# Kernel tuning notes

Measured on AMD Instinct MI355X. Metric: run time of the kernel, lower is better.

The kernel has to match this reference:

```python
import jax, jax.numpy as jnp
import numpy as np

D_MODEL = 512
KEY_DIM = 512
VALUE_DIM = 512
N_HEADS = 8


def setup_inputs() -> dict:
    key = jax.random.key(0)
    ks = jax.random.split(key, 12)
    B, S = 8, 1024
    s = 0.02
    return {
        "input1": jax.random.normal(ks[0], (B, S, D_MODEL), jnp.float32),
        "input2": jax.random.normal(ks[1], (B, S, D_MODEL), jnp.float32),
        "input3": jax.random.normal(ks[2], (B, S, D_MODEL), jnp.float32),
        # per-head projection weights stacked over heads: [H, D, d]
        "Wq": jax.random.normal(ks[3], (N_HEADS, D_MODEL, KEY_DIM), jnp.float32) * s,
        "bq": jnp.zeros((N_HEADS, KEY_DIM), jnp.float32),
        "Wk": jax.random.normal(ks[4], (N_HEADS, D_MODEL, KEY_DIM), jnp.float32) * s,
        "bk": jnp.zeros((N_HEADS, KEY_DIM), jnp.float32),
        "Wv": jax.random.normal(ks[5], (N_HEADS, D_MODEL, VALUE_DIM), jnp.float32) * s,
        "bv": jnp.zeros((N_HEADS, VALUE_DIM), jnp.float32),
        # output projection: concat of heads (H*VALUE_DIM) -> KEY_DIM
        "Wo": jax.random.normal(ks[6], (N_HEADS * VALUE_DIM, KEY_DIM), jnp.float32) * s,
        "bo": jnp.zeros((KEY_DIM,), jnp.float32),
    }


def reference(input1, input2, input3, Wq, bq, Wk, bk, Wv, bv, Wo, bo):
    # Batched equivalent of the per-head Python loop:
    # each head: q=Dense_q(input1), k=Dense_k(input2), v=Dense_v(input3);
    # softmax(q k^T / sqrt(key_dim)) v; concat over heads; Dense w_o.
    q = jnp.einsum("bsd,hde->bhse", input1, Wq) + bq[None, :, None, :]
    k = jnp.einsum("bsd,hde->bhse", input2, Wk) + bk[None, :, None, :]
    v = jnp.einsum("bsd,hde->bhse", input3, Wv) + bv[None, :, None, :]
    scale = 1.0 / jnp.sqrt(jnp.asarray(KEY_DIM, q.dtype))
    scores = jnp.einsum("bhqe,bhke->bhqk", q, k) * scale  # [B,H,S,S]
    attn = jax.nn.softmax(scores, axis=-1)
    heads = jnp.einsum("bhqk,bhke->bhqe", attn, v)  # [B,H,S,VALUE_DIM]
    B, H, S, E = heads.shape
    concat = jnp.transpose(heads, (0, 2, 1, 3)).reshape(B, S, H * E)
    return concat @ Wo + bo
```

## Files before the change

kernel.cpp:

```cpp
#include <hip/hip_runtime.h>
#include <hip/hip_bf16.h>

#define DEV static __device__ __forceinline__

typedef float f32x4 __attribute__((ext_vector_type(4)));
typedef __bf16 b16x8 __attribute__((ext_vector_type(8)));

DEV unsigned short f2bf(float f) {
  union { __hip_bfloat16 h; unsigned short u; } cv;
  cv.h = __float2bfloat16(f);
  return cv.u;
}

DEV void gload_lds16(const unsigned short* g, unsigned short* l) {
  __builtin_amdgcn_global_load_lds(
      (__attribute__((address_space(1))) void*)g,
      (__attribute__((address_space(3))) void*)l, 16, 0, 0);
}

__global__ __launch_bounds__(256) void k_conv_bf16(const float* __restrict__ src,
                                                   unsigned short* __restrict__ dst,
                                                   long long n4) {
  long long i = (long long)blockIdx.x * 256 + threadIdx.x;
  if (i >= n4) return;
  const float4 v = ((const float4*)src)[i];
  ushort4 o;
  o.x = f2bf(v.x); o.y = f2bf(v.y); o.z = f2bf(v.z); o.w = f2bf(v.w);
  ((ushort4*)dst)[i] = o;
}

__global__ __launch_bounds__(256) void k_transpose_bf16(const float* __restrict__ src,
                                                        unsigned short* __restrict__ dst,
                                                        int R, int C) {
  __shared__ float t[32][33];
  const long long zo = (long long)blockIdx.z * R * C;
  const int c0 = blockIdx.x * 32, r0 = blockIdx.y * 32;
  const int tx = threadIdx.x, ty = threadIdx.y;
#pragma unroll
  for (int i = 0; i < 4; ++i)
    t[ty + i * 8][tx] = src[zo + (long long)(r0 + ty + i * 8) * C + c0 + tx];
  __syncthreads();
#pragma unroll
  for (int i = 0; i < 4; ++i)
    dst[zo + (long long)(c0 + ty + i * 8) * R + r0 + tx] = f2bf(t[tx][ty + i * 8]);
}

__global__ __launch_bounds__(256) void k_uv(const float* __restrict__ Wq, const float* __restrict__ bk,
                                            const float* __restrict__ Wk, const float* __restrict__ bq,
                                            float* __restrict__ u, float* __restrict__ v) {
  const int sel = blockIdx.y;
  const float* W = sel ? Wk : Wq;
  const float* bb = sel ? bq : bk;
  float* dst = sel ? v : u;
  const int wave = threadIdx.x >> 6, lane = threadIdx.x & 63;
  const int idx = blockIdx.x * 4 + wave;
  const int h = idx >> 9, d = idx & 511;
  const float* wr = W + ((long long)h * 512 + d) * 512 + lane * 8;
  const float* br = bb + h * 512 + lane * 8;
  float s = 0.f;
#pragma unroll
  for (int k = 0; k < 8; ++k) s += wr[k] * br[k];
#pragma unroll
  for (int off = 32; off; off >>= 1) s += __shfl_xor(s, off);
  if (lane == 0) dst[h * 512 + d] = s;
}

__global__ __launch_bounds__(512) void k_bdot(const float* __restrict__ bq,
                                              const float* __restrict__ bk,
                                              float* __restrict__ c) {
  const int wave = threadIdx.x >> 6, lane = threadIdx.x & 63;
  const float* a = bq + wave * 512 + lane * 8;
  const float* b = bk + wave * 512 + lane * 8;
  float s = 0.f;
#pragma unroll
  for (int k = 0; k < 8; ++k) s += a[k] * b[k];
#pragma unroll
  for (int off = 32; off; off >>= 1) s += __shfl_xor(s, off);
  if (lane == 0) c[wave] = s;
}

__global__ __launch_bounds__(256) void k_rtct(const float* __restrict__ in1, const float* __restrict__ in2,
                                              const float* __restrict__ u, const float* __restrict__ v,
                                              const float* __restrict__ cbuf,
                                              float* __restrict__ rt, float* __restrict__ ct) {
  const int sel = blockIdx.y;
  const float* src = sel ? in2 : in1;
  const float* vec = sel ? v : u;
  float* dst = sel ? ct : rt;
  const int row = blockIdx.x;
  __shared__ float x[512];
  const float* p = src + (long long)row * 512;
  x[threadIdx.x] = p[threadIdx.x];
  x[threadIdx.x + 256] = p[threadIdx.x + 256];
  __syncthreads();
  const int wave = threadIdx.x >> 6, lane = threadIdx.x & 63;
  const int b = row >> 10, i = row & 1023;
#pragma unroll
  for (int t = 0; t < 2; ++t) {
    const int h = wave * 2 + t;
    const float* wv = vec + h * 512;
    float s = 0.f;
#pragma unroll
    for (int k = 0; k < 8; ++k) s += x[lane + k * 64] * wv[lane + k * 64];
#pragma unroll
    for (int off = 32; off; off >>= 1) s += __shfl_xor(s, off);
    if (lane == 0)
      dst[((long long)(b * 8 + h)) * 1024 + i] = s + (sel ? 0.f : cbuf[h]);
  }
}

__global__ __launch_bounds__(256) void k_softmax_bf16(unsigned short* __restrict__ P) {
  const int wave = threadIdx.x >> 6, lane = threadIdx.x & 63;
  unsigned short* p = P + ((long long)blockIdx.x * 4 + wave) * 1024 + lane * 16;
  const b16x8 v0 = *(const b16x8*)p;
  const b16x8 v1 = *(const b16x8*)(p + 8);
  float f[16];
#pragma unroll
  for (int j = 0; j < 8; ++j) { f[j] = (float)v0[j]; f[8 + j] = (float)v1[j]; }
  float mx = f[0];
#pragma unroll
  for (int j = 1; j < 16; ++j) mx = fmaxf(mx, f[j]);
#pragma unroll
  for (int off = 32; off; off >>= 1) mx = fmaxf(mx, __shfl_xor(mx, off));
  float sum = 0.f;
#pragma unroll
  for (int j = 0; j < 16; ++j) { f[j] = __expf(f[j] - mx); sum += f[j]; }
#pragma unroll
  for (int off = 32; off; off >>= 1) sum += __shfl_xor(sum, off);
  const float inv = 1.f / sum;
  b16x8 o0, o1;
#pragma unroll
  for (int j = 0; j < 8; ++j) { o0[j] = (__bf16)(f[j] * inv); o1[j] = (__bf16)(f[8 + j] * inv); }
  *(b16x8*)p = o0;
  *(b16x8*)(p + 8) = o1;
}

template <int OM>
__global__ __launch_bounds__(256) void k_gemm_bt(
    const unsigned short* __restrict__ A, const unsigned short* __restrict__ Bt,
    void* __restrict__ Cv, const float* __restrict__ bias,
    const float* __restrict__ rAdd, const float* __restrict__ cAdd,
    int K, int lda, int ldb, int ldc,
    int azs, int azm, long long azr,
    int bzs, int bzm, long long bzr,
    int czs, long long czr, int czm, int czc,
    int biasm, int bstr, int rstr, float scale) {
  __shared__ unsigned short lA[128 * 64];
  __shared__ unsigned short lB[128 * 64];
  const int tid = threadIdx.x, wave = tid >> 6, lane = tid & 63;
  const int z = blockIdx.z;
  const int m0 = blockIdx.y * 128, n0 = blockIdx.x * 128;
  const unsigned short* Az = A + (long long)((z >> azs) & azm) * azr + (long long)m0 * lda;
  const unsigned short* Bz = Bt + (long long)((z >> bzs) & bzm) * bzr + (long long)n0 * ldb;

  const int srow = wave * 32 + (lane >> 3);
  const int scol = (lane & 7) * 8;
  const unsigned short* ga = Az + (long long)srow * lda + scol;
  const unsigned short* gb = Bz + (long long)srow * ldb + scol;
  unsigned short* laBase = &lA[(wave * 32) * 64];
  unsigned short* lbBase = &lB[(wave * 32) * 64];

  f32x4 acc[4][4] = {};
  const int wr = (wave >> 1) * 64, wc = (wave & 1) * 64;
  const int fr = lane & 15, kq = (lane >> 4) * 8;

  for (int k0 = 0; k0 < K; k0 += 64) {
#pragma unroll
    for (int i = 0; i < 4; ++i) {
      gload_lds16(ga + (long long)(i * 8) * lda + k0, laBase + (i * 8) * 64);
      gload_lds16(gb + (long long)(i * 8) * ldb + k0, lbBase + (i * 8) * 64);
    }
    __syncthreads();
#pragma unroll
    for (int kk = 0; kk < 64; kk += 32) {
      b16x8 af[4], bf[4];
#pragma unroll
      for (int i = 0; i < 4; ++i)
        af[i] = *(const b16x8*)&lA[(wr + i * 16 + fr) * 64 + kk + kq];
#pragma unroll
      for (int j = 0; j < 4; ++j)
        bf[j] = *(const b16x8*)&lB[(wc + j * 16 + fr) * 64 + kk + kq];
#pragma unroll
      for (int i = 0; i < 4; ++i)
#pragma unroll
        for (int j = 0; j < 4; ++j)
          acc[i][j] = __builtin_amdgcn_mfma_f32_16x16x32_bf16(af[i], bf[j], acc[i][j], 0, 0, 0);
    }
    __syncthreads();
  }

  const long long coff = (long long)(z >> czs) * czr + (long long)(z & czm) * czc;
  const long long zr = (long long)z * rstr;
  const int rr = (lane >> 4) * 4;
#pragma unroll
  for (int j = 0; j < 4; ++j) {
    const int col = n0 + wc + j * 16 + fr;
    const float bval = bias ? bias[(long long)(z & biasm) * bstr + col] : 0.f;
    const float ca = cAdd ? cAdd[zr + col] : 0.f;
#pragma unroll
    for (int i = 0; i < 4; ++i) {
#pragma unroll
      for (int r = 0; r < 4; ++r) {
        const int row = m0 + wr + i * 16 + rr + r;
        const float ra = rAdd ? rAdd[zr + row] : 0.f;
        const float val = (acc[i][j][r] + ra + ca) * scale + bval;
        if constexpr (OM == 1) {
          ((unsigned short*)Cv)[coff + (long long)row * ldc + col] = f2bf(val);
        } else if constexpr (OM == 2) {
          ((unsigned short*)Cv)[coff + (long long)col * ldc + row] = f2bf(val);
        } else {
          ((float*)Cv)[coff + (long long)row * ldc + col] = val;
        }
      }
    }
  }
}

#define STAGE_A8(nb, koff, i)                                  \
  gload_lds16(gaL + (long long)((i) * 8) * lda + (koff) + scol, \
              &sh[nb][(wid * 32 + (i) * 8) * 64])
#define STAGE_B8(nb, koff, i)                                  \
  gload_lds16(gbL + (long long)((i) * 8) * ldb + (koff) + scol, \
              &sh[2 + (nb)][(wid * 32 + (i) * 8) * 64])

template <int OM>
__global__ __launch_bounds__(512, 2) void k_gemm8p(
    const unsigned short* __restrict__ A, const unsigned short* __restrict__ Bt,
    void* __restrict__ Cv, const float* __restrict__ bias,
    const float* __restrict__ rAdd, const float* __restrict__ cAdd,
    int K, int lda, int ldb, int ldc,
    int azs, int azm, long long azr,
    int bzs, int bzm, long long bzr,
    int czs, long long czr, int czm, int czc,
    int biasm, int bstr, int rstr, float scale, int kzm, int kzr) {
  __shared__ unsigned short sh[4][256 * 64];
  const int tid = threadIdx.x, wid = tid >> 6, lane = tid & 63;
  const int wm = wid >> 2, wn = wid & 3;

  const int gx = gridDim.x, gy = gridDim.y;
  const int nwg = gx * gy * gridDim.z;
  const int bidL = blockIdx.x + gx * (blockIdx.y + gy * blockIdx.z);
  const int q8 = nwg >> 3;
  const int idx = (bidL & 7) * q8 + (bidL >> 3);
  const int bx = idx % gx;
  const int rem = idx / gx;
  const int by = rem % gy;
  const int z = rem / gy;

  const int m0 = by * 256, n0 = bx * 256;
  const int kstart = (z & kzm) * kzr;
  const unsigned short* Az = A + (long long)((z >> azs) & azm) * azr + (long long)m0 * lda + kstart;
  const unsigned short* Bz = Bt + (long long)((z >> bzs) & bzm) * bzr + (long long)n0 * ldb + kstart;

  const int scol = (((lane & 7) ^ ((lane >> 3) & 7)) << 3);
  const unsigned short* gaL = Az + (long long)(wid * 32 + (lane >> 3)) * lda;
  const unsigned short* gbL = Bz + (long long)(wid * 32 + (lane >> 3)) * ldb;

  const int fr = lane & 15, kq = (lane >> 4) * 8;
  const int fsw = (fr & 7) << 3;
  const int rc0 = kq ^ fsw;
  const int rc1 = (32 + kq) ^ fsw;
  const int aBase = (wm * 128 + fr) * 64;
  const int bBase = (wn * 64 + fr) * 64;

  f32x4 acc[8][4] = {};
  b16x8 afr[4][2], bfr[4][2];
  const int NT = K >> 6;

#pragma unroll
  for (int i = 0; i < 4; ++i) { STAGE_A8(0, 0, i); STAGE_B8(0, 0, i); }

  for (int kt = 0; kt < NT; ++kt) {
    const int cur = kt & 1, nb = cur ^ 1;
    if (kt + 1 < NT) {
      const int ko = (kt + 1) << 6;
#pragma unroll
      for (int i = 0; i < 4; ++i) { STAGE_A8(nb, ko, i); STAGE_B8(nb, ko, i); }
      asm volatile("s_waitcnt vmcnt(8)" ::: "memory");
    } else {
      asm volatile("s_waitcnt vmcnt(0)" ::: "memory");
    }
    __builtin_amdgcn_s_barrier();
    __builtin_amdgcn_sched_barrier(0);

#pragma unroll
    for (int i = 0; i < 4; ++i) {
      afr[i][0] = *(const b16x8*)&sh[cur][aBase + i * 1024 + rc0];
      afr[i][1] = *(const b16x8*)&sh[cur][aBase + i * 1024 + rc1];
    }
#pragma unroll
    for (int j = 0; j < 2; ++j) {
      bfr[j][0] = *(const b16x8*)&sh[2 + cur][bBase + j * 1024 + rc0];
      bfr[j][1] = *(const b16x8*)&sh[2 + cur][bBase + j * 1024 + rc1];
    }
    __builtin_amdgcn_s_setprio(1);
#pragma unroll
    for (int t = 0; t < 2; ++t)
#pragma unroll
      for (int i = 0; i < 4; ++i)
#pragma unroll
        for (int j = 0; j < 2; ++j)
          acc[i][j] = __builtin_amdgcn_mfma_f32_16x16x32_bf16(afr[i][t], bfr[j][t], acc[i][j], 0, 0, 0);
    __builtin_amdgcn_s_setprio(0);
#pragma unroll
    for (int j = 2; j < 4; ++j) {
      bfr[j][0] = *(const b16x8*)&sh[2 + cur][bBase + j * 1024 + rc0];
      bfr[j][1] = *(const b16x8*)&sh[2 + cur][bBase + j * 1024 + rc1];
    }
    __builtin_amdgcn_s_setprio(1);
#pragma unroll
    for (int t = 0; t < 2; ++t)
#pragma unroll
      for (int i = 0; i < 4; ++i)
#pragma unroll
        for (int j = 2; j < 4; ++j)
          acc[i][j] = __builtin_amdgcn_mfma_f32_16x16x32_bf16(afr[i][t], bfr[j][t], acc[i][j], 0, 0, 0);
    __builtin_amdgcn_s_setprio(0);
#pragma unroll
    for (int i = 0; i < 4; ++i) {
      afr[i][0] = *(const b16x8*)&sh[cur][aBase + (i + 4) * 1024 + rc0];
      afr[i][1] = *(const b16x8*)&sh[cur][aBase + (i + 4) * 1024 + rc1];
    }
    __builtin_amdgcn_s_setprio(1);
#pragma unroll
    for (int t = 0; t < 2; ++t)
#pragma unroll
      for (int i = 0; i < 4; ++i)
#pragma unroll
        for (int j = 0; j < 2; ++j)
          acc[i + 4][j] = __builtin_amdgcn_mfma_f32_16x16x32_bf16(afr[i][t], bfr[j][t], acc[i + 4][j], 0, 0, 0);
    __builtin_amdgcn_s_setprio(0);
    __builtin_amdgcn_s_setprio(1);
#pragma unroll
    for (int t = 0; t < 2; ++t)
#pragma unroll
      for (int i = 0; i < 4; ++i)
#pragma unroll
        for (int j = 2; j < 4; ++j)
          acc[i + 4][j] = __builtin_amdgcn_mfma_f32_16x16x32_bf16(afr[i][t], bfr[j][t], acc[i + 4][j], 0, 0, 0);
    __builtin_amdgcn_s_setprio(0);

    __builtin_amdgcn_s_barrier();
  }

  const long long coff = (long long)(z >> czs) * czr + (long long)(z & czm) * czc;
  const long long zr = (long long)z * rstr;
  const int rr = (lane >> 4) * 4;
  unsigned short* flat = &sh[0][0];

  if constexpr (OM == 1 || OM == 2) {
#pragma unroll
    for (int j = 0; j < 4; ++j) {
      const int col = n0 + wn * 64 + j * 16 + fr;
      const float bval = bias ? bias[(long long)(z & biasm) * bstr + col] : 0.f;
      const float ca = cAdd ? cAdd[zr + col] : 0.f;
#pragma unroll
      for (int i = 0; i < 8; ++i) {
#pragma unroll
        for (int r = 0; r < 4; ++r) {
          const int row = m0 + wm * 128 + i * 16 + rr + r;
          const float ra = rAdd ? rAdd[zr + row] : 0.f;
          const float val = (acc[i][j][r] + ra + ca) * scale + bval;
          const int rowL = wm * 128 + i * 16 + rr + r;
          const int colL = wn * 64 + j * 16 + fr;
          const int sR = (OM == 2) ? colL : rowL;
          const int sC = (OM == 2) ? rowL : colL;
          flat[sR * 256 + (sC ^ ((sR & 7) << 3))] = f2bf(val);
        }
      }
    }
    __builtin_amdgcn_s_barrier();
    const long long rbase = (OM == 2) ? (long long)n0 : (long long)m0;
    const long long cbase = (OM == 2) ? (long long)m0 : (long long)n0;
    unsigned short* Cb = (unsigned short*)Cv;
#pragma unroll
    for (int it = 0; it < 16; ++it) {
      const int t = it * 512 + tid;
      const int R = t >> 5;
      const int Cq = t & 31;
      const int q = Cq ^ (R & 7);
      const b16x8 v = *(const b16x8*)&flat[R * 256 + q * 8];
      *(b16x8*)(Cb + coff + (rbase + R) * ldc + cbase + Cq * 8) = v;
    }
  } else {
    float* fflat = (float*)flat;
    float* Cf = (float*)Cv;
#pragma unroll
    for (int half = 0; half < 2; ++half) {
      if (wm == half) {
#pragma unroll
        for (int j = 0; j < 4; ++j) {
          const int col = n0 + wn * 64 + j * 16 + fr;
          const float bval = bias ? bias[(long long)(z & biasm) * bstr + col] : 0.f;
          const float ca = cAdd ? cAdd[zr + col] : 0.f;
#pragma unroll
          for (int i = 0; i < 8; ++i) {
#pragma unroll
            for (int r = 0; r < 4; ++r) {
              const int row = m0 + wm * 128 + i * 16 + rr + r;
              const float ra = rAdd ? rAdd[zr + row] : 0.f;
              const float val = (acc[i][j][r] + ra + ca) * scale + bval;
              const int Rl = i * 16 + rr + r;
              const int Cl = wn * 64 + j * 16 + fr;
              fflat[Rl * 256 + (Cl ^ ((Rl & 7) << 2))] = val;
            }
          }
        }
      }
      __builtin_amdgcn_s_barrier();
#pragma unroll
      for (int it = 0; it < 16; ++it) {
        const int t = it * 512 + tid;
        const int R = t >> 6;
        const int Cq = t & 63;
        const int q = Cq ^ (R & 7);
        const float4 v = *(const float4*)&fflat[R * 256 + q * 4];
        *(float4*)(Cf + coff + (long long)(m0 + half * 128 + R) * ldc + n0 + Cq * 4) = v;
      }
      __builtin_amdgcn_s_barrier();
    }
  }
}

__global__ __launch_bounds__(256) void k_reduce4(const float* __restrict__ p,
                                                 const float* __restrict__ bo,
                                                 float* __restrict__ out) {
  const long long i = (long long)blockIdx.x * 256 + threadIdx.x;
  const float4* p4 = (const float4*)p;
  float4 a = p4[i], b = p4[i + 1048576], c = p4[i + 2097152], d = p4[i + 3145728];
  const float4 bb = ((const float4*)bo)[i & 127];
  float4 o;
  o.x = a.x + b.x + c.x + d.x + bb.x;
  o.y = a.y + b.y + c.y + d.y + bb.y;
  o.z = a.z + b.z + c.z + d.z + bb.z;
  o.w = a.w + b.w + c.w + d.w + bb.w;
  ((float4*)out)[i] = o;
}

extern "C" void kernel_launch(void* const* d_in, const int* in_sizes, int n_in,
                              void* d_out, int out_size, void* d_ws, size_t ws_size,
                              hipStream_t stream) {
  const float* in1 = (const float*)d_in[0];
  const float* in2 = (const float*)d_in[1];
  const float* in3 = (const float*)d_in[2];
  const float* Wq = (const float*)d_in[3];
  const float* bq = (const float*)d_in[4];
  const float* Wk = (const float*)d_in[5];
  const float* bk = (const float*)d_in[6];
  const float* Wv = (const float*)d_in[7];
  const float* bv = (const float*)d_in[8];
  const float* Wo = (const float*)d_in[9];
  const float* bo = (const float*)d_in[10];

  const long long MB = 1024 * 1024;
  typedef unsigned short us;
  unsigned char* w = (unsigned char*)d_ws;
  us* in2b = (us*)(w);
  us* Tbuf = (us*)(w + 8 * MB);
  us* Vt = (us*)(w + 72 * MB);
  us* wvt = (us*)(w + 136 * MB);
  us* wot = (us*)(w + 140 * MB);
  us* scb = (us*)(w + 144 * MB);
  us* in1b = (us*)(w + 208 * MB);
  us* in3b = (us*)(w + 216 * MB);
  us* wqb = (us*)(w + 224 * MB);
  us* wkb = (us*)(w + 228 * MB);
  us* Gt = (us*)(w + 232 * MB);
  float* rt = (float*)(w + 236 * MB);
  float* ct = (float*)(w + 236 * MB + (256 << 10));
  float* ubuf = (float*)(w + 237 * MB);
  float* vbuf = (float*)(w + 237 * MB + (16 << 10));
  float* cbuf = (float*)(w + 237 * MB + (32 << 10));
  float* partials = (float*)(w + 72 * MB);
  if ((long long)ws_size < 238 * MB) return;

  const float iscale = 0.04419417382415922f;
  const long long SD = 1024 * 512;

  k_conv_bf16<<<4096, 256, 0, stream>>>(in1, in1b, 1048576);
  k_conv_bf16<<<4096, 256, 0, stream>>>(in2, in2b, 1048576);
  k_conv_bf16<<<4096, 256, 0, stream>>>(in3, in3b, 1048576);
  k_conv_bf16<<<2048, 256, 0, stream>>>(Wq, wqb, 524288);
  k_conv_bf16<<<2048, 256, 0, stream>>>(Wk, wkb, 524288);
  k_transpose_bf16<<<dim3(16, 16, 8), dim3(32, 8), 0, stream>>>(Wv, wvt, 512, 512);
  k_transpose_bf16<<<dim3(16, 128, 1), dim3(32, 8), 0, stream>>>(Wo, wot, 4096, 512);

  k_uv<<<dim3(1024, 2), 256, 0, stream>>>(Wq, bk, Wk, bq, ubuf, vbuf);
  k_bdot<<<1, 512, 0, stream>>>(bq, bk, cbuf);
  k_rtct<<<dim3(8192, 2), 256, 0, stream>>>(in1, in2, ubuf, vbuf, cbuf, rt, ct);

  k_gemm_bt<1><<<dim3(4, 4, 8), 256, 0, stream>>>(
      wkb, wqb, Gt, nullptr, nullptr, nullptr, 512, 512, 512, 512,
      0, 7, 262144LL, 0, 7, 262144LL, 0, 262144LL, 0, 0, 0, 0, 0, 1.f);

  k_gemm8p<1><<<dim3(2, 4, 64), 512, 0, stream>>>(
      in1b, Gt, Tbuf, nullptr, nullptr, nullptr, 512, 512, 512, 512,
      3, 7, SD, 0, 7, 262144LL, 0, SD, 0, 0, 0, 0, 0, 1.f, 0, 0);

  k_gemm8p<2><<<dim3(2, 4, 64), 512, 0, stream>>>(
      in3b, wvt, Vt, bv, nullptr, nullptr, 512, 512, 512, 1024,
      3, 7, SD, 0, 7, 262144LL, 0, SD, 0, 0, 7, 512, 0, 1.f, 0, 0);

  for (int c = 0; c < 2; ++c) {
    k_gemm8p<1><<<dim3(4, 4, 32), 512, 0, stream>>>(
        Tbuf + (long long)c * 32 * SD, in2b + (long long)c * 4 * SD, scb, nullptr,
        rt + c * 32768, ct + c * 32768, 512, 512, 512, 1024,
        0, 31, SD, 3, 3, SD, 0, 1048576LL, 0, 0, 0, 0, 1024, iscale, 0, 0);
    k_softmax_bf16<<<8192, 256, 0, stream>>>(scb);
    k_gemm8p<1><<<dim3(2, 4, 32), 512, 0, stream>>>(
        scb, Vt + (long long)c * 32 * SD, Tbuf + (long long)c * 16777216LL, nullptr,
        nullptr, nullptr, 1024, 1024, 1024, 4096,
        0, 31, 1048576LL, 0, 31, SD, 3, 4194304LL, 7, 512, 0, 0, 0, 1.f, 0, 0);
  }

  k_gemm8p<0><<<dim3(2, 32, 4), 512, 0, stream>>>(
      Tbuf, wot, partials, nullptr, nullptr, nullptr, 1024, 4096, 4096, 512,
      0, 0, 0, 0, 0, 0, 0, 4194304LL, 0, 0, 0, 0, 0, 1.f, 3, 1024);
  k_reduce4<<<4096, 256, 0, stream>>>(partials, bo, (float*)d_out);
}
```

Measured before the change: 481.5 us.

## Fold Wo into per-head value projection and fuse PV with output projection

```diff
diff --git a/kernel.cpp b/kernel.cpp
--- a/kernel.cpp
+++ b/kernel.cpp
@@ -107,6 +107,24 @@
     if (lane == 0)
       dst[((long long)(b * 8 + h)) * 1024 + i] = s + (sel ? 0.f : cbuf[h]);
   }
+}
+
+__global__ __launch_bounds__(256) void k_bvo(const float* __restrict__ Wo,
+                                             const float* __restrict__ bv,
+                                             float* __restrict__ bvo) {
+  const int h = blockIdx.x;
+  __shared__ float bs[512];
+  bs[threadIdx.x] = bv[h * 512 + threadIdx.x];
+  bs[threadIdx.x + 256] = bv[h * 512 + threadIdx.x + 256];
+  __syncthreads();
+  float a0 = 0.f, a1 = 0.f;
+  for (int e = 0; e < 512; ++e) {
+    const float* row = Wo + ((long long)(h * 512 + e)) * 512;
+    a0 += bs[e] * row[threadIdx.x];
+    a1 += bs[e] * row[threadIdx.x + 256];
+  }
+  bvo[h * 512 + threadIdx.x] = a0;
+  bvo[h * 512 + threadIdx.x + 256] = a1;
 }
 
 __global__ __launch_bounds__(256) void k_softmax_bf16(unsigned short* __restrict__ P) {
@@ -422,18 +440,18 @@
   }
 }
 
-__global__ __launch_bounds__(256) void k_reduce4(const float* __restrict__ p,
+__global__ __launch_bounds__(256) void k_reduce8(const float* __restrict__ p,
                                                  const float* __restrict__ bo,
                                                  float* __restrict__ out) {
   const long long i = (long long)blockIdx.x * 256 + threadIdx.x;
   const float4* p4 = (const float4*)p;
-  float4 a = p4[i], b = p4[i + 1048576], c = p4[i + 2097152], d = p4[i + 3145728];
   const float4 bb = ((const float4*)bo)[i & 127];
-  float4 o;
-  o.x = a.x + b.x + c.x + d.x + bb.x;
-  o.y = a.y + b.y + c.y + d.y + bb.y;
-  o.z = a.z + b.z + c.z + d.z + bb.z;
-  o.w = a.w + b.w + c.w + d.w + bb.w;
+  float4 o = bb;
+#pragma unroll
+  for (int ks = 0; ks < 8; ++ks) {
+    const float4 v = p4[i + (long long)ks * 524288];
+    o.x += v.x; o.y += v.y; o.z += v.z; o.w += v.w;
+  }
   ((float4*)out)[i] = o;
 }
 
@@ -455,23 +473,25 @@
   const long long MB = 1024 * 1024;
   typedef unsigned short us;
   unsigned char* w = (unsigned char*)d_ws;
-  us* in2b = (us*)(w);
-  us* Tbuf = (us*)(w + 8 * MB);
-  us* Vt = (us*)(w + 72 * MB);
-  us* wvt = (us*)(w + 136 * MB);
-  us* wot = (us*)(w + 140 * MB);
-  us* scb = (us*)(w + 144 * MB);
-  us* in1b = (us*)(w + 208 * MB);
-  us* in3b = (us*)(w + 216 * MB);
-  us* wqb = (us*)(w + 224 * MB);
-  us* wkb = (us*)(w + 228 * MB);
+  us* scb = (us*)(w);
+  float* partials = (float*)(w + 64 * MB);
+  us* Ubuf = (us*)(w + 128 * MB);
+  us* Tc = (us*)(w + 160 * MB);
+  us* in1b = (us*)(w + 192 * MB);
+  us* in2b = (us*)(w + 200 * MB);
+  us* in3b = (us*)(w + 208 * MB);
+  us* wqb = (us*)(w + 216 * MB);
+  us* wkb = (us*)(w + 220 * MB);
+  us* wvb = (us*)(w + 224 * MB);
+  us* wotb = (us*)(w + 228 * MB);
   us* Gt = (us*)(w + 232 * MB);
+  us* Wvot = (us*)(w + 216 * MB);
   float* rt = (float*)(w + 236 * MB);
   float* ct = (float*)(w + 236 * MB + (256 << 10));
-  float* ubuf = (float*)(w + 237 * MB);
-  float* vbuf = (float*)(w + 237 * MB + (16 << 10));
-  float* cbuf = (float*)(w + 237 * MB + (32 << 10));
-  float* partials = (float*)(w + 72 * MB);
+  float* ubuf = (float*)(w + 236 * MB + (512 << 10));
+  float* vbuf = (float*)(w + 236 * MB + (528 << 10));
+  float* cbuf = (float*)(w + 236 * MB + (544 << 10));
+  float* bvo = (float*)(w + 236 * MB + (560 << 10));
   if ((long long)ws_size < 238 * MB) return;
 
   const float iscale = 0.04419417382415922f;
@@ -482,8 +502,8 @@
   k_conv_bf16<<<4096, 256, 0, stream>>>(in3, in3b, 1048576);
   k_conv_bf16<<<2048, 256, 0, stream>>>(Wq, wqb, 524288);
   k_conv_bf16<<<2048, 256, 0, stream>>>(Wk, wkb, 524288);
-  k_transpose_bf16<<<dim3(16, 16, 8), dim3(32, 8), 0, stream>>>(Wv, wvt, 512, 512);
-  k_transpose_bf16<<<dim3(16, 128, 1), dim3(32, 8), 0, stream>>>(Wo, wot, 4096, 512);
+  k_conv_bf16<<<2048, 256, 0, stream>>>(Wv, wvb, 524288);
+  k_transpose_bf16<<<dim3(16, 128, 1), dim3(32, 8), 0, stream>>>(Wo, wotb, 4096, 512);
 
   k_uv<<<dim3(1024, 2), 256, 0, stream>>>(Wq, bk, Wk, bq, ubuf, vbuf);
   k_bdot<<<1, 512, 0, stream>>>(bq, bk, cbuf);
@@ -493,28 +513,27 @@
       wkb, wqb, Gt, nullptr, nullptr, nullptr, 512, 512, 512, 512,
       0, 7, 262144LL, 0, 7, 262144LL, 0, 262144LL, 0, 0, 0, 0, 0, 1.f);
 
-  k_gemm8p<1><<<dim3(2, 4, 64), 512, 0, stream>>>(
-      in1b, Gt, Tbuf, nullptr, nullptr, nullptr, 512, 512, 512, 512,
-      3, 7, SD, 0, 7, 262144LL, 0, SD, 0, 0, 0, 0, 0, 1.f, 0, 0);
-
-  k_gemm8p<2><<<dim3(2, 4, 64), 512, 0, stream>>>(
-      in3b, wvt, Vt, bv, nullptr, nullptr, 512, 512, 512, 1024,
-      3, 7, SD, 0, 7, 262144LL, 0, SD, 0, 0, 7, 512, 0, 1.f, 0, 0);
+  k_gemm_bt<1><<<dim3(4, 4, 8), 256, 0, stream>>>(
+      wotb, wvb, Wvot, nullptr, nullptr, nullptr, 512, 4096, 512, 512,
+      0, 7, 512LL, 0, 7, 262144LL, 0, 262144LL, 0, 0, 0, 0, 0, 1.f);
+  k_bvo<<<8, 256, 0, stream>>>(Wo, bv, bvo);
 
   for (int c = 0; c < 2; ++c) {
+    const long long cSD = (long long)c * 4 * SD;
+    k_gemm8p<1><<<dim3(2, 4, 32), 512, 0, stream>>>(
+        in1b + cSD, Gt, Tc, nullptr, nullptr, nullptr, 512, 512, 512, 512,
+        3, 3, SD, 0, 7, 262144LL, 0, SD, 0, 0, 0, 0, 0, 1.f, 0, 0);
+    k_gemm8p<2><<<dim3(2, 4, 32), 512, 0, stream>>>(
+        in3b + cSD, Wvot, Ubuf, bvo, nullptr, nullptr, 512, 512, 512, 8192,
+        3, 3, SD, 0, 7, 262144LL, 3, 4194304LL, 7, 1024, 7, 512, 0, 1.f, 0, 0);
     k_gemm8p<1><<<dim3(4, 4, 32), 512, 0, stream>>>(
-        Tbuf + (long long)c * 32 * SD, in2b + (long long)c * 4 * SD, scb, nullptr,
-        rt + c * 32768, ct + c * 32768, 512, 512, 512, 1024,
-        0, 31, SD, 3, 3, SD, 0, 1048576LL, 0, 0, 0, 0, 1024, iscale, 0, 0);
+        Tc, in2b + cSD, scb, nullptr,
+        rt + c * 32768, ct + c * 32768, 512, 512, 512, 8192,
+        0, 31, SD, 3, 3, SD, 3, 8388608LL, 7, 1024, 0, 0, 1024, iscale, 0, 0);
     k_softmax_bf16<<<8192, 256, 0, stream>>>(scb);
-    k_gemm8p<1><<<dim3(2, 4, 32), 512, 0, stream>>>(
-        scb, Vt + (long long)c * 32 * SD, Tbuf + (long long)c * 16777216LL, nullptr,
-        nullptr, nullptr, 1024, 1024, 1024, 4096,
-        0, 31, 1048576LL, 0, 31, SD, 3, 4194304LL, 7, 512, 0, 0, 0, 1.f, 0, 0);
-  }
-
-  k_gemm8p<0><<<dim3(2, 32, 4), 512, 0, stream>>>(
-      Tbuf, wot, partials, nullptr, nullptr, nullptr, 1024, 4096, 4096, 512,
-      0, 0, 0, 0, 0, 0, 0, 4194304LL, 0, 0, 0, 0, 0, 1.f, 3, 1024);
-  k_reduce4<<<4096, 256, 0, stream>>>(partials, bo, (float*)d_out);
-}
+    k_gemm8p<0><<<dim3(2, 4, 32), 512, 0, stream>>>(
+        scb, Ubuf, partials, nullptr, nullptr, nullptr, 1024, 8192, 8192, 512,
+        3, 3, 8388608LL, 3, 3, 4194304LL, 3, 524288LL, 7, 2097152, 0, 0, 0, 1.f, 7, 1024);
+    k_reduce8<<<2048, 256, 0, stream>>>(partials, bo, (float*)d_out + (long long)c * 2097152);
+  }
+}
```

Result: slower. 516.4 us (+7.3%).

## Add 128x256 BK32 double-buffered GEMM kernel for projection and attention GEMMs

Applied to the files above, without the earlier changes.

```diff
diff --git a/kernel.cpp b/kernel.cpp
--- a/kernel.cpp
+++ b/kernel.cpp
@@ -216,6 +216,143 @@
   }
 }
 
+template <int OM>
+__global__ __launch_bounds__(512, 4) void k_g32(
+    const unsigned short* __restrict__ A, const unsigned short* __restrict__ Bt,
+    void* __restrict__ Cv, const float* __restrict__ bias,
+    const float* __restrict__ rAdd, const float* __restrict__ cAdd,
+    int K, int lda, int ldb, int ldc,
+    int azs, int azm, long long azr,
+    int bzs, int bzm, long long bzr,
+    int czs, long long czr, int czm, int czc,
+    int biasm, int bstr, int rstr, float scale) {
+  __shared__ unsigned short sh[24576];
+  const int tid = threadIdx.x, wid = tid >> 6, lane = tid & 63;
+  const int wm = wid >> 2, wn = wid & 3;
+
+  const int gx = gridDim.x, gy = gridDim.y;
+  const int nwg = gx * gy * gridDim.z;
+  const int bidL = blockIdx.x + gx * (blockIdx.y + gy * blockIdx.z);
+  const int q8 = nwg >> 3;
+  const int idx = (bidL & 7) * q8 + (bidL >> 3);
+  const int bx = idx % gx;
+  const int rem = idx / gx;
+  const int by = rem % gy;
+  const int z = rem / gy;
+
+  const int m0 = by * 128, n0 = bx * 256;
+  const unsigned short* Az = A + (long long)((z >> azs) & azm) * azr + (long long)m0 * lda;
+  const unsigned short* Bz = Bt + (long long)((z >> bzs) & bzm) * bzr + (long long)n0 * ldb;
+
+  const int scol = (((lane & 3) ^ ((lane >> 2) & 3)) << 3);
+  const unsigned short* gaL = Az + (long long)(wid * 16 + (lane >> 2)) * lda + scol;
+  const unsigned short* gbL = Bz + (long long)(wid * 32 + (lane >> 2)) * ldb + scol;
+
+  const int fr = lane & 15;
+  const int rq = ((lane >> 4) ^ (fr & 3)) << 3;
+  f32x4 acc[4][4] = {};
+  b16x8 afr[4], bfr[4];
+  const int NT = K >> 5;
+
+  gload_lds16(gaL, &sh[(wid * 16) * 32]);
+  gload_lds16(gbL, &sh[8192 + (wid * 32) * 32]);
+  gload_lds16(gbL + (long long)16 * ldb, &sh[8192 + (wid * 32 + 16) * 32]);
+
+  for (int kt = 0; kt < NT; ++kt) {
+    const int cur = kt & 1, nb = cur ^ 1;
+    if (kt + 1 < NT) {
+      const int ko = (kt + 1) << 5;
+      gload_lds16(gaL + ko, &sh[nb * 4096 + (wid * 16) * 32]);
+      gload_lds16(gbL + ko, &sh[8192 + nb * 8192 + (wid * 32) * 32]);
+      gload_lds16(gbL + (long long)16 * ldb + ko, &sh[8192 + nb * 8192 + (wid * 32 + 16) * 32]);
+      asm volatile("s_waitcnt vmcnt(3)" ::: "memory");
+    } else {
+      asm volatile("s_waitcnt vmcnt(0)" ::: "memory");
+    }
+    __builtin_amdgcn_s_barrier();
+    __builtin_amdgcn_sched_barrier(0);
+
+    const int aO = cur * 4096, bO = 8192 + cur * 8192;
+#pragma unroll
+    for (int i = 0; i < 4; ++i)
+      afr[i] = *(const b16x8*)&sh[aO + (wm * 64 + i * 16 + fr) * 32 + rq];
+#pragma unroll
+    for (int j = 0; j < 4; ++j)
+      bfr[j] = *(const b16x8*)&sh[bO + (wn * 64 + j * 16 + fr) * 32 + rq];
+    __builtin_amdgcn_s_setprio(1);
+#pragma unroll
+    for (int i = 0; i < 4; ++i)
+#pragma unroll
+      for (int j = 0; j < 4; ++j)
+        acc[i][j] = __builtin_amdgcn_mfma_f32_16x16x32_bf16(afr[i], bfr[j], acc[i][j], 0, 0, 0);
+    __builtin_amdgcn_s_setprio(0);
+
+    __builtin_amdgcn_s_barrier();
+  }
+
+  const long long coff = (long long)(z >> czs) * czr + (long long)(z & czm) * czc;
+  const long long zr = (long long)z * rstr;
+  const int rr = (lane >> 4) * 4;
+  unsigned short* flat = &sh[0];
+  unsigned short* Cb = (unsigned short*)Cv;
+  const long long rbase = (OM == 2) ? (long long)n0 : (long long)m0;
+  const long long cbase = (OM == 2) ? (long long)m0 : (long long)n0;
+
+#pragma unroll
+  for (int half = 0; half < 2; ++half) {
+    const bool mine = (OM == 2) ? ((wn >> 1) == half) : (wm == half);
+    if (mine) {
+#pragma unroll
+      for (int j = 0; j < 4; ++j) {
+        const int col = n0 + wn * 64 + j * 16 + fr;
+        const float bval = bias ? bias[(long long)(z & biasm) * bstr + col] : 0.f;
+        const float ca = cAdd ? cAdd[zr + col] : 0.f;
+#pragma unroll
+        for (int i = 0; i < 4; ++i) {
+#pragma unroll
+          for (int r = 0; r < 4; ++r) {
+            const int row = m0 + wm * 64 + i * 16 + rr + r;
+            const float ra = rAdd ? rAdd[zr + row] : 0.f;
+            const float val = (acc[i][j][r] + ra + ca) * scale + bval;
+            const int rowL = wm * 64 + i * 16 + rr + r;
+            const int colL = wn * 64 + j * 16 + fr;
+            if constexpr (OM == 2) {
+              const int lR = colL - half * 128;
+              flat[lR * 128 + (rowL ^ ((lR & 7) << 3))] = f2bf(val);
+            } else {
+              const int lR = rowL - half * 64;
+              flat[lR * 256 + (colL ^ ((lR & 7) << 3))] = f2bf(val);
+            }
+          }
+        }
+      }
+    }
+    __builtin_amdgcn_s_barrier();
+    if constexpr (OM == 2) {
+#pragma unroll
+      for (int it = 0; it < 4; ++it) {
+        const int t = it * 512 + tid;
+        const int R = t >> 4;
+        const int Cq = t & 15;
+        const int q = Cq ^ (R & 7);
+        const b16x8 v = *(const b16x8*)&flat[R * 128 + q * 8];
+        *(b16x8*)(Cb + coff + (rbase + half * 128 + R) * ldc + cbase + Cq * 8) = v;
+      }
+    } else {
+#pragma unroll
+      for (int it = 0; it < 4; ++it) {
+        const int t = it * 512 + tid;
+        const int R = t >> 5;
+        const int Cq = t & 31;
+        const int q = Cq ^ (R & 7);
+        const b16x8 v = *(const b16x8*)&flat[R * 256 + q * 8];
+        *(b16x8*)(Cb + coff + (rbase + half * 64 + R) * ldc + cbase + Cq * 8) = v;
+      }
+    }
+    __builtin_amdgcn_s_barrier();
+  }
+}
+
 #define STAGE_A8(nb, koff, i)                                  \
   gload_lds16(gaL + (long long)((i) * 8) * lda + (koff) + scol, \
               &sh[nb][(wid * 32 + (i) * 8) * 64])
@@ -346,79 +483,41 @@
   const long long coff = (long long)(z >> czs) * czr + (long long)(z & czm) * czc;
   const long long zr = (long long)z * rstr;
   const int rr = (lane >> 4) * 4;
-  unsigned short* flat = &sh[0][0];
-
-  if constexpr (OM == 1 || OM == 2) {
-#pragma unroll
-    for (int j = 0; j < 4; ++j) {
-      const int col = n0 + wn * 64 + j * 16 + fr;
-      const float bval = bias ? bias[(long long)(z & biasm) * bstr + col] : 0.f;
-      const float ca = cAdd ? cAdd[zr + col] : 0.f;
-#pragma unroll
-      for (int i = 0; i < 8; ++i) {
-#pragma unroll
-        for (int r = 0; r < 4; ++r) {
-          const int row = m0 + wm * 128 + i * 16 + rr + r;
-          const float ra = rAdd ? rAdd[zr + row] : 0.f;
-          const float val = (acc[i][j][r] + ra + ca) * scale + bval;
-          const int rowL = wm * 128 + i * 16 + rr + r;
-          const int colL = wn * 64 + j * 16 + fr;
-          const int sR = (OM == 2) ? colL : rowL;
-          const int sC = (OM == 2) ? rowL : colL;
-          flat[sR * 256 + (sC ^ ((sR & 7) << 3))] = f2bf(val);
-        }
-      }
-    }
-    __builtin_amdgcn_s_barrier();
-    const long long rbase = (OM == 2) ? (long long)n0 : (long long)m0;
-    const long long cbase = (OM == 2) ? (long long)m0 : (long long)n0;
-    unsigned short* Cb = (unsigned short*)Cv;
-#pragma unroll
-    for (int it = 0; it < 16; ++it) {
-      const int t = it * 512 + tid;
-      const int R = t >> 5;
-      const int Cq = t & 31;
-      const int q = Cq ^ (R & 7);
-      const b16x8 v = *(const b16x8*)&flat[R * 256 + q * 8];
-      *(b16x8*)(Cb + coff + (rbase + R) * ldc + cbase + Cq * 8) = v;
-    }
-  } else {
-    float* fflat = (float*)flat;
-    float* Cf = (float*)Cv;
-#pragma unroll
-    for (int half = 0; half < 2; ++half) {
-      if (wm == half) {
-#pragma unroll
-        for (int j = 0; j < 4; ++j) {
-          const int col = n0 + wn * 64 + j * 16 + fr;
-          const float bval = bias ? bias[(long long)(z & biasm) * bstr + col] : 0.f;
-          const float ca = cAdd ? cAdd[zr + col] : 0.f;
-#pragma unroll
-          for (int i = 0; i < 8; ++i) {
-#pragma unroll
-            for (int r = 0; r < 4; ++r) {
-              const int row = m0 + wm * 128 + i * 16 + rr + r;
-              const float ra = rAdd ? rAdd[zr + row] : 0.f;
-              const float val = (acc[i][j][r] + ra + ca) * scale + bval;
-              const int Rl = i * 16 + rr + r;
-              const int Cl = wn * 64 + j * 16 + fr;
-              fflat[Rl * 256 + (Cl ^ ((Rl & 7) << 2))] = val;
-            }
+  float* fflat = (float*)&sh[0][0];
+  float* Cf = (float*)Cv;
+#pragma unroll
+  for (int half = 0; half < 2; ++half) {
+    if (wm == half) {
+#pragma unroll
+      for (int j = 0; j < 4; ++j) {
+        const int col = n0 + wn * 64 + j * 16 + fr;
+        const float bval = bias ? bias[(long long)(z & biasm) * bstr + col] : 0.f;
+        const float ca = cAdd ? cAdd[zr + col] : 0.f;
+#pragma unroll
+        for (int i = 0; i < 8; ++i) {
+#pragma unroll
+          for (int r = 0; r < 4; ++r) {
+            const int row = m0 + wm * 128 + i * 16 + rr + r;
+            const float ra = rAdd ? rAdd[zr + row] : 0.f;
+            const float val = (acc[i][j][r] + ra + ca) * scale + bval;
+            const int Rl = i * 16 + rr + r;
+            const int Cl = wn * 64 + j * 16 + fr;
+            fflat[Rl * 256 + (Cl ^ ((Rl & 7) << 2))] = val;
           }
         }
       }
-      __builtin_amdgcn_s_barrier();
-#pragma unroll
-      for (int it = 0; it < 16; ++it) {
-        const int t = it * 512 + tid;
-        const int R = t >> 6;
-        const int Cq = t & 63;
-        const int q = Cq ^ (R & 7);
-        const float4 v = *(const float4*)&fflat[R * 256 + q * 4];
-        *(float4*)(Cf + coff + (long long)(m0 + half * 128 + R) * ldc + n0 + Cq * 4) = v;
-      }
-      __builtin_amdgcn_s_barrier();
-    }
+    }
+    __builtin_amdgcn_s_barrier();
+#pragma unroll
+    for (int it = 0; it < 16; ++it) {
+      const int t = it * 512 + tid;
+      const int R = t >> 6;
+      const int Cq = t & 63;
+      const int q = Cq ^ (R & 7);
+      const float4 v = *(const float4*)&fflat[R * 256 + q * 4];
+      *(float4*)(Cf + coff + (long long)(m0 + half * 128 + R) * ldc + n0 + Cq * 4) = v;
+    }
+    __builtin_amdgcn_s_barrier();
   }
 }
 
@@ -493,24 +592,24 @@
       wkb, wqb, Gt, nullptr, nullptr, nullptr, 512, 512, 512, 512,
       0, 7, 262144LL, 0, 7, 262144LL, 0, 262144LL, 0, 0, 0, 0, 0, 1.f);
 
-  k_gemm8p<1><<<dim3(2, 4, 64), 512, 0, stream>>>(
+  k_g32<1><<<dim3(2, 8, 64), 512, 0, stream>>>(
       in1b, Gt, Tbuf, nullptr, nullptr, nullptr, 512, 512, 512, 512,
-      3, 7, SD, 0, 7, 262144LL, 0, SD, 0, 0, 0, 0, 0, 1.f, 0, 0);
-
-  k_gemm8p<2><<<dim3(2, 4, 64), 512, 0, stream>>>(
+      3, 7, SD, 0, 7, 262144LL, 0, SD, 0, 0, 0, 0, 0, 1.f);
+
+  k_g32<2><<<dim3(2, 8, 64), 512, 0, stream>>>(
       in3b, wvt, Vt, bv, nullptr, nullptr, 512, 512, 512, 1024,
-      3, 7, SD, 0, 7, 262144LL, 0, SD, 0, 0, 7, 512, 0, 1.f, 0, 0);
+      3, 7, SD, 0, 7, 262144LL, 0, SD, 0, 0, 7, 512, 0, 1.f);
 
   for (int c = 0; c < 2; ++c) {
-    k_gemm8p<1><<<dim3(4, 4, 32), 512, 0, stream>>>(
+    k_g32<1><<<dim3(4, 8, 32), 512, 0, stream>>>(
         Tbuf + (long long)c * 32 * SD, in2b + (long long)c * 4 * SD, scb, nullptr,
         rt + c * 32768, ct + c * 32768, 512, 512, 512, 1024,
-        0, 31, SD, 3, 3, SD, 0, 1048576LL, 0, 0, 0, 0, 1024, iscale, 0, 0);
+        0, 31, SD, 3, 3, SD, 0, 1048576LL, 0, 0, 0, 0, 1024, iscale);
     k_softmax_bf16<<<8192, 256, 0, stream>>>(scb);
-    k_gemm8p<1><<<dim3(2, 4, 32), 512, 0, stream>>>(
+    k_g32<1><<<dim3(2, 8, 32), 512, 0, stream>>>(
         scb, Vt + (long long)c * 32 * SD, Tbuf + (long long)c * 16777216LL, nullptr,
         nullptr, nullptr, 1024, 1024, 1024, 4096,
-        0, 31, 1048576LL, 0, 31, SD, 3, 4194304LL, 7, 512, 0, 0, 0, 1.f, 0, 0);
+        0, 31, 1048576LL, 0, 31, SD, 3, 4194304LL, 7, 512, 0, 0, 0, 1.f);
   }
 
   k_gemm8p<0><<<dim3(2, 32, 4), 512, 0, stream>>>(
```

Result: slower. 509.0 us (+5.7%).

## Fuse conversion launches and replace split-K output GEMM with 128x128 kernel

Applied to the files above, without the earlier changes.

```diff
diff --git a/kernel.cpp b/kernel.cpp
--- a/kernel.cpp
+++ b/kernel.cpp
@@ -18,24 +18,50 @@
       (__attribute__((address_space(3))) void*)l, 16, 0, 0);
 }
 
-__global__ __launch_bounds__(256) void k_conv_bf16(const float* __restrict__ src,
-                                                   unsigned short* __restrict__ dst,
-                                                   long long n4) {
-  long long i = (long long)blockIdx.x * 256 + threadIdx.x;
-  if (i >= n4) return;
+__global__ __launch_bounds__(256) void k_convall(
+    const float* __restrict__ in1, const float* __restrict__ in2,
+    const float* __restrict__ in3, const float* __restrict__ Wq,
+    const float* __restrict__ Wk,
+    unsigned short* __restrict__ in1b, unsigned short* __restrict__ in2b,
+    unsigned short* __restrict__ in3b, unsigned short* __restrict__ wqb,
+    unsigned short* __restrict__ wkb) {
+  const int b = blockIdx.x;
+  const float* src;
+  unsigned short* dst;
+  long long off;
+  if (b < 4096) { src = in1; dst = in1b; off = b; }
+  else if (b < 8192) { src = in2; dst = in2b; off = b - 4096; }
+  else if (b < 12288) { src = in3; dst = in3b; off = b - 8192; }
+  else if (b < 14336) { src = Wq; dst = wqb; off = b - 12288; }
+  else { src = Wk; dst = wkb; off = b - 14336; }
+  const long long i = off * 256 + threadIdx.x;
   const float4 v = ((const float4*)src)[i];
   ushort4 o;
   o.x = f2bf(v.x); o.y = f2bf(v.y); o.z = f2bf(v.z); o.w = f2bf(v.w);
   ((ushort4*)dst)[i] = o;
 }
 
-__global__ __launch_bounds__(256) void k_transpose_bf16(const float* __restrict__ src,
-                                                        unsigned short* __restrict__ dst,
-                                                        int R, int C) {
+__global__ __launch_bounds__(256) void k_transall(const float* __restrict__ Wv,
+                                                  const float* __restrict__ Wo,
+                                                  unsigned short* __restrict__ wvt,
+                                                  unsigned short* __restrict__ wot) {
   __shared__ float t[32][33];
-  const long long zo = (long long)blockIdx.z * R * C;
-  const int c0 = blockIdx.x * 32, r0 = blockIdx.y * 32;
-  const int tx = threadIdx.x, ty = threadIdx.y;
+  const int yy = blockIdx.y;
+  const float* src;
+  unsigned short* dst;
+  long long zo;
+  int R, C, r0;
+  const int c0 = blockIdx.x * 32;
+  if (yy < 128) {
+    src = Wv; dst = wvt; R = 512; C = 512;
+    zo = (long long)(yy >> 4) * 512 * 512;
+    r0 = (yy & 15) * 32;
+  } else {
+    src = Wo; dst = wot; R = 4096; C = 512;
+    zo = 0;
+    r0 = (yy - 128) * 32;
+  }
+  const int tx = threadIdx.x & 31, ty = threadIdx.x >> 5;
 #pragma unroll
   for (int i = 0; i < 4; ++i)
     t[ty + i * 8][tx] = src[zo + (long long)(r0 + ty + i * 8) * C + c0 + tx];
@@ -348,6 +374,134 @@
   const int rr = (lane >> 4) * 4;
   unsigned short* flat = &sh[0][0];
 
+#pragma unroll
+  for (int j = 0; j < 4; ++j) {
+    const int col = n0 + wn * 64 + j * 16 + fr;
+    const float bval = bias ? bias[(long long)(z & biasm) * bstr + col] : 0.f;
+    const float ca = cAdd ? cAdd[zr + col] : 0.f;
+#pragma unroll
+    for (int i = 0; i < 8; ++i) {
+#pragma unroll
+      for (int r = 0; r < 4; ++r) {
+        const int row = m0 + wm * 128 + i * 16 + rr + r;
+        const float ra = rAdd ? rAdd[zr + row] : 0.f;
+        const float val = (acc[i][j][r] + ra + ca) * scale + bval;
+        const int rowL = wm * 128 + i * 16 + rr + r;
+        const int colL = wn * 64 + j * 16 + fr;
+        const int sR = (OM == 2) ? colL : rowL;
+        const int sC = (OM == 2) ? rowL : colL;
+        flat[sR * 256 + (sC ^ ((sR & 7) << 3))] = f2bf(val);
+      }
+    }
+  }
+  __builtin_amdgcn_s_barrier();
+  const long long rbase = (OM == 2) ? (long long)n0 : (long long)m0;
+  const long long cbase = (OM == 2) ? (long long)m0 : (long long)n0;
+  unsigned short* Cb = (unsigned short*)Cv;
+#pragma unroll
+  for (int it = 0; it < 16; ++it) {
+    const int t = it * 512 + tid;
+    const int R = t >> 5;
+    const int Cq = t & 31;
+    const int q = Cq ^ (R & 7);
+    const b16x8 v = *(const b16x8*)&flat[R * 256 + q * 8];
+    *(b16x8*)(Cb + coff + (rbase + R) * ldc + cbase + Cq * 8) = v;
+  }
+}
+
+#define STAGE_GA(nb, koff, i)                                  \
+  gload_lds16(gaL + (long long)((i) * 8) * lda + (koff) + scol, \
+              &sh[nb][(wid * 32 + (i) * 8) * 64])
+#define STAGE_GB(nb, koff, i)                                  \
+  gload_lds16(gbL + (long long)((i) * 8) * ldb + (koff) + scol, \
+              &sh[2 + (nb)][(wid * 32 + (i) * 8) * 64])
+
+template <int OM>
+__global__ __launch_bounds__(256, 2) void k_g128(
+    const unsigned short* __restrict__ A, const unsigned short* __restrict__ Bt,
+    void* __restrict__ Cv, const float* __restrict__ bias,
+    const float* __restrict__ rAdd, const float* __restrict__ cAdd,
+    int K, int lda, int ldb, int ldc,
+    int azs, int azm, long long azr,
+    int bzs, int bzm, long long bzr,
+    int czs, long long czr, int czm, int czc,
+    int biasm, int bstr, int rstr, float scale, int kzm, int kzr) {
+  __shared__ unsigned short sh[4][128 * 64];
+  const int tid = threadIdx.x, wid = tid >> 6, lane = tid & 63;
+  const int wm = wid >> 1, wn = wid & 1;
+
+  const int gx = gridDim.x, gy = gridDim.y;
+  const int nwg = gx * gy * gridDim.z;
+  const int bidL = blockIdx.x + gx * (blockIdx.y + gy * blockIdx.z);
+  const int q8 = nwg >> 3;
+  const int idx = (bidL & 7) * q8 + (bidL >> 3);
+  const int bx = idx % gx;
+  const int rem = idx / gx;
+  const int by = rem % gy;
+  const int z = rem / gy;
+
+  const int m0 = by * 128, n0 = bx * 128;
+  const int kstart = (z & kzm) * kzr;
+  const unsigned short* Az = A + (long long)((z >> azs) & azm) * azr + (long long)m0 * lda + kstart;
+  const unsigned short* Bz = Bt + (long long)((z >> bzs) & bzm) * bzr + (long long)n0 * ldb + kstart;
+
+  const int scol = (((lane & 7) ^ ((lane >> 3) & 7)) << 3);
+  const unsigned short* gaL = Az + (long long)(wid * 32 + (lane >> 3)) * lda;
+  const unsigned short* gbL = Bz + (long long)(wid * 32 + (lane >> 3)) * ldb;
+
+  const int fr = lane & 15, kq = (lane >> 4) * 8;
+  const int fsw = (fr & 7) << 3;
+  const int rc0 = kq ^ fsw;
+  const int rc1 = (32 + kq) ^ fsw;
+  const int aBase = (wm * 64 + fr) * 64;
+  const int bBase = (wn * 64 + fr) * 64;
+
+  f32x4 acc[4][4] = {};
+  b16x8 afr[4][2], bfr[4][2];
+  const int NT = K >> 6;
+
+#pragma unroll
+  for (int i = 0; i < 4; ++i) { STAGE_GA(0, 0, i); STAGE_GB(0, 0, i); }
+
+  for (int kt = 0; kt < NT; ++kt) {
+    const int cur = kt & 1, nb = cur ^ 1;
+    if (kt + 1 < NT) {
+      const int ko = (kt + 1) << 6;
+#pragma unroll
+      for (int i = 0; i < 4; ++i) { STAGE_GA(nb, ko, i); STAGE_GB(nb, ko, i); }
+      asm volatile("s_waitcnt vmcnt(8)" ::: "memory");
+    } else {
+      asm volatile("s_waitcnt vmcnt(0)" ::: "memory");
+    }
+    __builtin_amdgcn_s_barrier();
+    __builtin_amdgcn_sched_barrier(0);
+
+#pragma unroll
+    for (int i = 0; i < 4; ++i) {
+      afr[i][0] = *(const b16x8*)&sh[cur][aBase + i * 1024 + rc0];
+      afr[i][1] = *(const b16x8*)&sh[cur][aBase + i * 1024 + rc1];
+    }
+#pragma unroll
+    for (int j = 0; j < 4; ++j) {
+      bfr[j][0] = *(const b16x8*)&sh[2 + cur][bBase + j * 1024 + rc0];
+      bfr[j][1] = *(const b16x8*)&sh[2 + cur][bBase + j * 1024 + rc1];
+    }
+#pragma unroll
+    for (int t = 0; t < 2; ++t)
+#pragma unroll
+      for (int i = 0; i < 4; ++i)
+#pragma unroll
+        for (int j = 0; j < 4; ++j)
+          acc[i][j] = __builtin_amdgcn_mfma_f32_16x16x32_bf16(afr[i][t], bfr[j][t], acc[i][j], 0, 0, 0);
+
+    __builtin_amdgcn_s_barrier();
+  }
+
+  const long long coff = (long long)(z >> czs) * czr + (long long)(z & czm) * czc;
+  const long long zr = (long long)z * rstr;
+  const int rr = (lane >> 4) * 4;
+  unsigned short* flat = &sh[0][0];
+
   if constexpr (OM == 1 || OM == 2) {
 #pragma unroll
     for (int j = 0; j < 4; ++j) {
@@ -355,17 +509,17 @@
       const float bval = bias ? bias[(long long)(z & biasm) * bstr + col] : 0.f;
       const float ca = cAdd ? cAdd[zr + col] : 0.f;
 #pragma unroll
-      for (int i = 0; i < 8; ++i) {
+      for (int i = 0; i < 4; ++i) {
 #pragma unroll
         for (int r = 0; r < 4; ++r) {
-          const int row = m0 + wm * 128 + i * 16 + rr + r;
+          const int row = m0 + wm * 64 + i * 16 + rr + r;
           const float ra = rAdd ? rAdd[zr + row] : 0.f;
           const float val = (acc[i][j][r] + ra + ca) * scale + bval;
-          const int rowL = wm * 128 + i * 16 + rr + r;
+          const int rowL = wm * 64 + i * 16 + rr + r;
           const int colL = wn * 64 + j * 16 + fr;
           const int sR = (OM == 2) ? colL : rowL;
           const int sC = (OM == 2) ? rowL : colL;
-          flat[sR * 256 + (sC ^ ((sR & 7) << 3))] = f2bf(val);
+          flat[sR * 128 + (sC ^ ((sR & 7) << 3))] = f2bf(val);
         }
       }
     }
@@ -374,67 +528,46 @@
     const long long cbase = (OM == 2) ? (long long)m0 : (long long)n0;
     unsigned short* Cb = (unsigned short*)Cv;
 #pragma unroll
+    for (int it = 0; it < 8; ++it) {
+      const int t = it * 256 + tid;
+      const int R = t >> 4;
+      const int Cq = t & 15;
+      const int q = Cq ^ (R & 7);
+      const b16x8 v = *(const b16x8*)&flat[R * 128 + q * 8];
+      *(b16x8*)(Cb + coff + (rbase + R) * ldc + cbase + Cq * 8) = v;
+    }
+  } else {
+    float* fflat = (float*)flat;
+    float* Cf = (float*)Cv;
+#pragma unroll
+    for (int j = 0; j < 4; ++j) {
+      const int col = n0 + wn * 64 + j * 16 + fr;
+      const float bval = bias ? bias[(long long)(z & biasm) * bstr + col] : 0.f;
+      const float ca = cAdd ? cAdd[zr + col] : 0.f;
+#pragma unroll
+      for (int i = 0; i < 4; ++i) {
+#pragma unroll
+        for (int r = 0; r < 4; ++r) {
+          const int row = m0 + wm * 64 + i * 16 + rr + r;
+          const float ra = rAdd ? rAdd[zr + row] : 0.f;
+          const float val = (acc[i][j][r] + ra + ca) * scale + bval;
+          const int Rl = wm * 64 + i * 16 + rr + r;
+          const int Cl = wn * 64 + j * 16 + fr;
+          fflat[Rl * 128 + (Cl ^ ((Rl & 7) << 2))] = val;
+        }
+      }
+    }
+    __builtin_amdgcn_s_barrier();
+#pragma unroll
     for (int it = 0; it < 16; ++it) {
-      const int t = it * 512 + tid;
+      const int t = it * 256 + tid;
       const int R = t >> 5;
       const int Cq = t & 31;
       const int q = Cq ^ (R & 7);
-      const b16x8 v = *(const b16x8*)&flat[R * 256 + q * 8];
-      *(b16x8*)(Cb + coff + (rbase + R) * ldc + cbase + Cq * 8) = v;
-    }
-  } else {
-    float* fflat = (float*)flat;
-    float* Cf = (float*)Cv;
-#pragma unroll
-    for (int half = 0; half < 2; ++half) {
-      if (wm == half) {
-#pragma unroll
-        for (int j = 0; j < 4; ++j) {
-          const int col = n0 + wn * 64 + j * 16 + fr;
-          const float bval = bias ? bias[(long long)(z & biasm) * bstr + col] : 0.f;
-          const float ca = cAdd ? cAdd[zr + col] : 0.f;
-#pragma unroll
-          for (int i = 0; i < 8; ++i) {
-#pragma unroll
-            for (int r = 0; r < 4; ++r) {
-              const int row = m0 + wm * 128 + i * 16 + rr + r;
-              const float ra = rAdd ? rAdd[zr + row] : 0.f;
-              const float val = (acc[i][j][r] + ra + ca) * scale + bval;
-              const int Rl = i * 16 + rr + r;
-              const int Cl = wn * 64 + j * 16 + fr;
-              fflat[Rl * 256 + (Cl ^ ((Rl & 7) << 2))] = val;
-            }
-          }
-        }
-      }
-      __builtin_amdgcn_s_barrier();
-#pragma unroll
-      for (int it = 0; it < 16; ++it) {
-        const int t = it * 512 + tid;
-        const int R = t >> 6;
-        const int Cq = t & 63;
-        const int q = Cq ^ (R & 7);
-        const float4 v = *(const float4*)&fflat[R * 256 + q * 4];
-        *(float4*)(Cf + coff + (long long)(m0 + half * 128 + R) * ldc + n0 + Cq * 4) = v;
-      }
-      __builtin_amdgcn_s_barrier();
-    }
-  }
-}
-
-__global__ __launch_bounds__(256) void k_reduce4(const float* __restrict__ p,
-                                                 const float* __restrict__ bo,
-                                                 float* __restrict__ out) {
-  const long long i = (long long)blockIdx.x * 256 + threadIdx.x;
-  const float4* p4 = (const float4*)p;
-  float4 a = p4[i], b = p4[i + 1048576], c = p4[i + 2097152], d = p4[i + 3145728];
-  const float4 bb = ((const float4*)bo)[i & 127];
-  float4 o;
-  o.x = a.x + b.x + c.x + d.x + bb.x;
-  o.y = a.y + b.y + c.y + d.y + bb.y;
-  o.z = a.z + b.z + c.z + d.z + bb.z;
-  o.w = a.w + b.w + c.w + d.w + bb.w;
-  ((float4*)out)[i] = o;
+      const float4 v = *(const float4*)&fflat[R * 128 + q * 4];
+      *(float4*)(Cf + coff + (long long)(m0 + R) * ldc + n0 + Cq * 4) = v;
+    }
+  }
 }
 
 extern "C" void kernel_launch(void* const* d_in, const int* in_sizes, int n_in,
@@ -471,19 +604,14 @@
   float* ubuf = (float*)(w + 237 * MB);
   float* vbuf = (float*)(w + 237 * MB + (16 << 10));
   float* cbuf = (float*)(w + 237 * MB + (32 << 10));
-  float* partials = (float*)(w + 72 * MB);
   if ((long long)ws_size < 238 * MB) return;
 
   const float iscale = 0.04419417382415922f;
   const long long SD = 1024 * 512;
 
-  k_conv_bf16<<<4096, 256, 0, stream>>>(in1, in1b, 1048576);
-  k_conv_bf16<<<4096, 256, 0, stream>>>(in2, in2b, 1048576);
-  k_conv_bf16<<<4096, 256, 0, stream>>>(in3, in3b, 1048576);
-  k_conv_bf16<<<2048, 256, 0, stream>>>(Wq, wqb, 524288);
-  k_conv_bf16<<<2048, 256, 0, stream>>>(Wk, wkb, 524288);
-  k_transpose_bf16<<<dim3(16, 16, 8), dim3(32, 8), 0, stream>>>(Wv, wvt, 512, 512);
-  k_transpose_bf16<<<dim3(16, 128, 1), dim3(32, 8), 0, stream>>>(Wo, wot, 4096, 512);
+  k_convall<<<16384, 256, 0, stream>>>(in1, in2, in3, Wq, Wk,
+                                       in1b, in2b, in3b, wqb, wkb);
+  k_transall<<<dim3(16, 256), 256, 0, stream>>>(Wv, Wo, wvt, wot);
 
   k_uv<<<dim3(1024, 2), 256, 0, stream>>>(Wq, bk, Wk, bq, ubuf, vbuf);
   k_bdot<<<1, 512, 0, stream>>>(bq, bk, cbuf);
@@ -513,8 +641,7 @@
         0, 31, 1048576LL, 0, 31, SD, 3, 4194304LL, 7, 512, 0, 0, 0, 1.f, 0, 0);
   }
 
-  k_gemm8p<0><<<dim3(2, 32, 4), 512, 0, stream>>>(
-      Tbuf, wot, partials, nullptr, nullptr, nullptr, 1024, 4096, 4096, 512,
-      0, 0, 0, 0, 0, 0, 0, 4194304LL, 0, 0, 0, 0, 0, 1.f, 3, 1024);
-  k_reduce4<<<4096, 256, 0, stream>>>(partials, bo, (float*)d_out);
-}
+  k_g128<0><<<dim3(4, 64, 1), 256, 0, stream>>>(
+      Tbuf, wot, d_out, bo, nullptr, nullptr, 4096, 4096, 4096, 512,
+      0, 0, 0, 0, 0, 0, 0, 0, 0, 0, 0, 0, 0, 1.f, 0, 0);
+}
```

After: 465.0 us. 3.4% less time.
